# Optimization experiments

Hardware: AMD Instinct MI355X
Metric: run time of the kernel (lower is better)

## Reference

```python
import jax, jax.numpy as jnp
import numpy as np


def setup_inputs() -> dict:
    key = jax.random.key(0)
    k1, k2, k3 = jax.random.split(key, 3)
    N, RANK, M = 1024, 16, 4096
    W = jax.random.normal(k1, (N, RANK), dtype=jnp.float32)
    H = jax.random.normal(k2, (RANK, M), dtype=jnp.float32)
    tau_tilde = jax.random.uniform(k3, (N, RANK), dtype=jnp.float32)
    return {"W": W, "H": H, "tau_tilde": tau_tilde}


def reference(W, H, tau_tilde):
    # W: (N, rank), H: (rank, M), tau_tilde: (N, rank)
    M = H.shape[1]
    Nf = M // 2 + 1
    # FFT of softplus(H), keep non-negative freqs, rebuild full spectrum by conjugate symmetry
    Hf = jnp.fft.fft(jax.nn.softplus(H), axis=1)[:, :Nf]            # (rank, Nf) complex
    Hf_reverse = Hf[:, 1:Nf - 1][:, ::-1]                            # flip of interior bins
    Hft = jnp.concatenate([Hf, jnp.conj(Hf_reverse)], axis=1)        # (rank, M)
    f = jnp.arange(M, dtype=jnp.float32) / M                         # (M,)
    # omega[N,d,M] = exp(-i 2 pi tau[N,d] f[M]); Wf = softplus(W)[...,None] * omega
    omega = jnp.exp(-2j * jnp.pi * (tau_tilde[:, :, None] * f[None, None, :]))
    Wf = jax.nn.softplus(W)[:, :, None].astype(omega.dtype) * omega  # (N, rank, M)
    V = jnp.einsum('NdM,dM->NM', Wf, Hft)                            # (N, M) complex
    return V
```

## Files before the change

kernel.cpp:

```cpp
#include <hip/hip_runtime.h>
#include <math.h>

#define MLEN 4096
#define RANK 16
#define NROWS 1024
#define TWO_PI 6.2831853071795864769f

__device__ float2 g_Hft[RANK * MLEN];

__device__ __forceinline__ float softplus_f(float x) {
    return fmaxf(x, 0.0f) + log1pf(__expf(-fabsf(x)));
}

__global__ __launch_bounds__(1024) void fft_rows_kernel(const float* __restrict__ H) {
    __shared__ float2 buf[MLEN];
    const int row = blockIdx.x;
    const int tid = threadIdx.x;
    const float* h = H + row * MLEN;

    for (int i = tid; i < MLEN; i += 1024) {
        int j = (int)(__brev((unsigned)i) >> 20);
        buf[j] = make_float2(softplus_f(h[i]), 0.0f);
    }
    __syncthreads();

    #pragma unroll
    for (int s = 0; s < 12; ++s) {
        const int half = 1 << s;
        const float inv_len = 1.0f / (float)(half << 1);
        for (int t = tid; t < MLEN / 2; t += 1024) {
            const int pos = t & (half - 1);
            const int i0  = ((t >> s) << (s + 1)) + pos;
            const int i1  = i0 + half;
            float sn, c;
            __sincosf(TWO_PI * ((float)pos * inv_len), &sn, &c);
            const float2 a = buf[i0];
            const float2 b = buf[i1];
            const float vre = c * b.x + sn * b.y;
            const float vim = c * b.y - sn * b.x;
            buf[i0] = make_float2(a.x + vre, a.y + vim);
            buf[i1] = make_float2(a.x - vre, a.y - vim);
        }
        __syncthreads();
    }

    for (int i = tid; i < MLEN; i += 1024) {
        g_Hft[row * MLEN + i] = buf[i];
    }
}

template <int MODE>
__global__ __launch_bounds__(256) void shiftnmf_mix_kernel(const float* __restrict__ W,
                                                           const float* __restrict__ tau,
                                                           float* __restrict__ out,
                                                           int out_size_floats) {
    __shared__ float sw_s[256];
    __shared__ float tau_s[256];

    const int tid = threadIdx.x;
    const int m   = blockIdx.x * 256 + tid;
    const int n0  = blockIdx.y * 16;

    sw_s[tid]  = softplus_f(W[n0 * RANK + tid]);
    tau_s[tid] = tau[n0 * RANK + tid];
    __syncthreads();

    float2 h[RANK];
    #pragma unroll
    for (int d = 0; d < RANK; ++d) h[d] = g_Hft[d * MLEN + m];

    const float fm = (float)m * (1.0f / (float)MLEN);

    #pragma unroll 1
    for (int ln = 0; ln < 16; ++ln) {
        float sw[RANK], tv[RANK];
        #pragma unroll
        for (int d = 0; d < RANK; ++d) {
            sw[d] = sw_s[ln * RANK + d];
            tv[d] = tau_s[ln * RANK + d];
        }

        float ar = 0.0f, ai = 0.0f;
        #pragma unroll
        for (int d = 0; d < RANK; ++d) {
            float s, c;
            __sincosf(TWO_PI * (tv[d] * fm), &s, &c);
            ar = fmaf(sw[d], fmaf(s, h[d].y, c * h[d].x), ar);
            if (MODE != 0) {
                ai = fmaf(sw[d], fmaf(c, h[d].y, -s * h[d].x), ai);
            }
        }
        const int nm = (n0 + ln) * MLEN + m;
        if (MODE == 0) {
            out[nm] = ar;
        } else if (MODE == 1) {
            out[2 * nm]     = ar;
            out[2 * nm + 1] = ai;
        } else {
            const long long fi = 2LL * nm;
            if (fi + 1 < (long long)out_size_floats) {
                out[fi]     = ar;
                out[fi + 1] = ai;
            }
        }
    }
}

extern "C" void kernel_launch(void* const* d_in, const int* in_sizes, int n_in,
                              void* d_out, int out_size, void* d_ws, size_t ws_size,
                              hipStream_t stream) {
    const float* W   = (const float*)d_in[0];
    const float* H   = (const float*)d_in[1];
    const float* tau = (const float*)d_in[2];
    float* out = (float*)d_out;
    (void)d_ws; (void)ws_size; (void)in_sizes; (void)n_in;

    fft_rows_kernel<<<dim3(RANK), dim3(1024), 0, stream>>>(H);

    const dim3 grid(MLEN / 256, NROWS / 16);
    if (out_size == NROWS * MLEN) {
        shiftnmf_mix_kernel<0><<<grid, dim3(256), 0, stream>>>(W, tau, out, out_size);
    } else if (out_size == 2 * NROWS * MLEN) {
        shiftnmf_mix_kernel<1><<<grid, dim3(256), 0, stream>>>(W, tau, out, out_size);
    } else {
        shiftnmf_mix_kernel<2><<<grid, dim3(256), 0, stream>>>(W, tau, out, out_size);
    }
}
```

Before: 94.61 us.

## Exploit conjugate symmetry to compute mirrored output columns, use radix-4 FFT

The real-output mixing kernel now computes column a and column M-a together. It uses the conjugate symmetry of the H spectrum and a per-(n,d) phase factor exp(-i2πτ) that is precomputed in shared memory, which roughly halves the sin/cos evaluations per output. The FFT stages are rewritten as radix-4 passes, halving the number of barriers, and sin/cos switch to the native amdgcn intrinsics that take revolutions. Rows per block drop to 8, and column 0 is handled separately by one thread per block; the extra phase multiply could add rounding error.

```diff
diff --git a/kernel.cpp b/kernel.cpp
--- a/kernel.cpp
+++ b/kernel.cpp
@@ -4,7 +4,7 @@
 #define MLEN 4096
 #define RANK 16
 #define NROWS 1024
-#define TWO_PI 6.2831853071795864769f
+#define LNB 8
 
 __device__ float2 g_Hft[RANK * MLEN];
 
@@ -15,93 +15,153 @@
 __global__ __launch_bounds__(1024) void fft_rows_kernel(const float* __restrict__ H) {
     __shared__ float2 buf[MLEN];
     const int row = blockIdx.x;
-    const int tid = threadIdx.x;
+    const int t   = threadIdx.x;
     const float* h = H + row * MLEN;
 
-    for (int i = tid; i < MLEN; i += 1024) {
+    for (int i = t; i < MLEN; i += 1024) {
         int j = (int)(__brev((unsigned)i) >> 20);
         buf[j] = make_float2(softplus_f(h[i]), 0.0f);
     }
     __syncthreads();
 
     #pragma unroll
-    for (int s = 0; s < 12; ++s) {
-        const int half = 1 << s;
-        const float inv_len = 1.0f / (float)(half << 1);
-        for (int t = tid; t < MLEN / 2; t += 1024) {
-            const int pos = t & (half - 1);
-            const int i0  = ((t >> s) << (s + 1)) + pos;
-            const int i1  = i0 + half;
-            float sn, c;
-            __sincosf(TWO_PI * ((float)pos * inv_len), &sn, &c);
-            const float2 a = buf[i0];
-            const float2 b = buf[i1];
-            const float vre = c * b.x + sn * b.y;
-            const float vim = c * b.y - sn * b.x;
-            buf[i0] = make_float2(a.x + vre, a.y + vim);
-            buf[i1] = make_float2(a.x - vre, a.y - vim);
-        }
+    for (int s = 0; s < 12; s += 2) {
+        const int h1 = 1 << s;
+        const int p  = t & (h1 - 1);
+        const int k  = ((t >> s) << (s + 2)) + p;
+        const float rA = (float)p * (1.0f / (float)(h1 << 2));
+        const float ca = __builtin_amdgcn_cosf(rA);
+        const float sa = __builtin_amdgcn_sinf(rA);
+        const float c1 = ca * ca - sa * sa;
+        const float s1 = 2.0f * ca * sa;
+
+        const float2 a0 = buf[k];
+        const float2 a1 = buf[k + h1];
+        const float2 a2 = buf[k + 2 * h1];
+        const float2 a3 = buf[k + 3 * h1];
+
+        const float2 w1a1 = make_float2(c1 * a1.x + s1 * a1.y, c1 * a1.y - s1 * a1.x);
+        const float2 w1a3 = make_float2(c1 * a3.x + s1 * a3.y, c1 * a3.y - s1 * a3.x);
+        const float2 u0 = make_float2(a0.x + w1a1.x, a0.y + w1a1.y);
+        const float2 u1 = make_float2(a0.x - w1a1.x, a0.y - w1a1.y);
+        const float2 u2 = make_float2(a2.x + w1a3.x, a2.y + w1a3.y);
+        const float2 u3 = make_float2(a2.x - w1a3.x, a2.y - w1a3.y);
+
+        const float2 wAu2 = make_float2(ca * u2.x + sa * u2.y, ca * u2.y - sa * u2.x);
+        const float2 v    = make_float2(ca * u3.x + sa * u3.y, ca * u3.y - sa * u3.x);
+        const float2 wBu3 = make_float2(v.y, -v.x);
+
+        buf[k]          = make_float2(u0.x + wAu2.x, u0.y + wAu2.y);
+        buf[k + h1]     = make_float2(u1.x + wBu3.x, u1.y + wBu3.y);
+        buf[k + 2 * h1] = make_float2(u0.x - wAu2.x, u0.y - wAu2.y);
+        buf[k + 3 * h1] = make_float2(u1.x - wBu3.x, u1.y - wBu3.y);
         __syncthreads();
     }
 
-    for (int i = tid; i < MLEN; i += 1024) {
+    for (int i = t; i < MLEN; i += 1024) {
         g_Hft[row * MLEN + i] = buf[i];
     }
 }
 
-template <int MODE>
-__global__ __launch_bounds__(256) void shiftnmf_mix_kernel(const float* __restrict__ W,
-                                                           const float* __restrict__ tau,
-                                                           float* __restrict__ out,
-                                                           int out_size_floats) {
+__global__ __launch_bounds__(256) void mix_mirror_kernel(const float* __restrict__ W,
+                                                         const float* __restrict__ tau,
+                                                         float* __restrict__ out) {
+    __shared__ __align__(16) float sw_s[LNB * RANK];
+    __shared__ __align__(16) float tv_s[LNB * RANK];
+    __shared__ __align__(16) float qc_s[LNB * RANK];
+    __shared__ __align__(16) float qi_s[LNB * RANK];
+
+    const int tid = threadIdx.x;
+    const int n0  = blockIdx.y * LNB;
+
+    if (tid < LNB * RANK) {
+        const float sw = softplus_f(W[n0 * RANK + tid]);
+        const float tv = tau[n0 * RANK + tid];
+        const float c2 = __builtin_amdgcn_cosf(tv);
+        const float s2 = __builtin_amdgcn_sinf(tv);
+        sw_s[tid] = sw;
+        tv_s[tid] = tv;
+        qc_s[tid] = sw * c2;
+        qi_s[tid] = -sw * s2;
+    }
+    __syncthreads();
+
+    const int a  = blockIdx.x * 256 + tid + 1;
+    const int mm = MLEN - a;
+    const float fa = (float)a * (1.0f / (float)MLEN);
+
+    float2 h[RANK];
+    #pragma unroll
+    for (int d = 0; d < RANK; ++d) h[d] = g_Hft[d * MLEN + a];
+
+    #pragma unroll 1
+    for (int ln = 0; ln < LNB; ++ln) {
+        const int base = ln * RANK;
+        float ar = 0.0f, aw = 0.0f;
+        #pragma unroll
+        for (int d = 0; d < RANK; ++d) {
+            const float tv = tv_s[base + d];
+            const float sw = sw_s[base + d];
+            const float qc = qc_s[base + d];
+            const float qi = qi_s[base + d];
+            const float r  = tv * fa;
+            const float c  = __builtin_amdgcn_cosf(r);
+            const float s  = __builtin_amdgcn_sinf(r);
+            const float tre = fmaf(s, h[d].y, c * h[d].x);
+            const float tim = fmaf(c, h[d].y, -s * h[d].x);
+            ar = fmaf(sw, tre, ar);
+            aw = fmaf(qc, tre, fmaf(qi, tim, aw));
+        }
+        const int rowbase = (n0 + ln) * MLEN;
+        out[rowbase + a]  = ar;
+        out[rowbase + mm] = aw;
+    }
+
+    if (blockIdx.x == 0 && tid == 0) {
+        float h0[RANK];
+        #pragma unroll
+        for (int d = 0; d < RANK; ++d) h0[d] = g_Hft[d * MLEN].x;
+        for (int ln = 0; ln < LNB; ++ln) {
+            float v = 0.0f;
+            #pragma unroll
+            for (int d = 0; d < RANK; ++d) v = fmaf(sw_s[ln * RANK + d], h0[d], v);
+            out[(n0 + ln) * MLEN] = v;
+        }
+    }
+}
+
+__global__ __launch_bounds__(256) void mix_generic_kernel(const float* __restrict__ W,
+                                                          const float* __restrict__ tau,
+                                                          float* __restrict__ out,
+                                                          int out_size_floats) {
     __shared__ float sw_s[256];
     __shared__ float tau_s[256];
-
     const int tid = threadIdx.x;
     const int m   = blockIdx.x * 256 + tid;
     const int n0  = blockIdx.y * 16;
-
     sw_s[tid]  = softplus_f(W[n0 * RANK + tid]);
     tau_s[tid] = tau[n0 * RANK + tid];
     __syncthreads();
-
     float2 h[RANK];
     #pragma unroll
     for (int d = 0; d < RANK; ++d) h[d] = g_Hft[d * MLEN + m];
-
     const float fm = (float)m * (1.0f / (float)MLEN);
-
     #pragma unroll 1
     for (int ln = 0; ln < 16; ++ln) {
-        float sw[RANK], tv[RANK];
-        #pragma unroll
-        for (int d = 0; d < RANK; ++d) {
-            sw[d] = sw_s[ln * RANK + d];
-            tv[d] = tau_s[ln * RANK + d];
-        }
-
         float ar = 0.0f, ai = 0.0f;
         #pragma unroll
         for (int d = 0; d < RANK; ++d) {
-            float s, c;
-            __sincosf(TWO_PI * (tv[d] * fm), &s, &c);
-            ar = fmaf(sw[d], fmaf(s, h[d].y, c * h[d].x), ar);
-            if (MODE != 0) {
-                ai = fmaf(sw[d], fmaf(c, h[d].y, -s * h[d].x), ai);
-            }
+            const float r = tau_s[ln * RANK + d] * fm;
+            const float c = __builtin_amdgcn_cosf(r);
+            const float s = __builtin_amdgcn_sinf(r);
+            const float sw = sw_s[ln * RANK + d];
+            ar = fmaf(sw, fmaf(s, h[d].y, c * h[d].x), ar);
+            ai = fmaf(sw, fmaf(c, h[d].y, -s * h[d].x), ai);
         }
-        const int nm = (n0 + ln) * MLEN + m;
-        if (MODE == 0) {
-            out[nm] = ar;
-        } else if (MODE == 1) {
-            out[2 * nm]     = ar;
-            out[2 * nm + 1] = ai;
-        } else {
-            const long long fi = 2LL * nm;
-            if (fi + 1 < (long long)out_size_floats) {
-                out[fi]     = ar;
-                out[fi + 1] = ai;
-            }
+        const long long fi = 2LL * ((long long)(n0 + ln) * MLEN + m);
+        if (fi + 1 < (long long)out_size_floats) {
+            out[fi]     = ar;
+            out[fi + 1] = ai;
         }
     }
 }
@@ -117,12 +177,10 @@
 
     fft_rows_kernel<<<dim3(RANK), dim3(1024), 0, stream>>>(H);
 
-    const dim3 grid(MLEN / 256, NROWS / 16);
     if (out_size == NROWS * MLEN) {
-        shiftnmf_mix_kernel<0><<<grid, dim3(256), 0, stream>>>(W, tau, out, out_size);
-    } else if (out_size == 2 * NROWS * MLEN) {
-        shiftnmf_mix_kernel<1><<<grid, dim3(256), 0, stream>>>(W, tau, out, out_size);
+        mix_mirror_kernel<<<dim3(8, NROWS / LNB), dim3(256), 0, stream>>>(W, tau, out);
     } else {
-        shiftnmf_mix_kernel<2><<<grid, dim3(256), 0, stream>>>(W, tau, out, out_size);
+        mix_generic_kernel<<<dim3(MLEN / 256, NROWS / 16), dim3(256), 0, stream>>>(
+            W, tau, out, out_size);
     }
 }
```

Measured after the change: 82.91 us. 1.14x faster.
